# Kernel optimization log

Hardware: AMD Instinct MI355X
Metric: run time of the kernel (lower is better)

Reference implementation:

```python
import jax, jax.numpy as jnp
import numpy as np

OUT = 7        # out_size (H and W bins)
OUT_D = 4      # out_size_depth (D bins)
SCALE = 0.125  # spatial_scale (HW)
SCALE_D = 0.25 # spatial_scale_depth
SN = 2         # sample_num per bin per axis


def setup_inputs() -> dict:
    key = jax.random.key(0)
    k1, k2, k3, k4, k5 = jax.random.split(key, 5)
    N, C, D, H, W = 2, 128, 24, 128, 128
    features = jax.random.normal(k1, (N, C, D, H, W), dtype=jnp.float32)
    R = 256
    b = jax.random.randint(k2, (R,), 0, N).astype(jnp.float32)
    xx = jnp.sort(jax.random.uniform(k3, (R, 2), minval=0.0, maxval=1023.0), axis=1)
    yy = jnp.sort(jax.random.uniform(k4, (R, 2), minval=0.0, maxval=1023.0), axis=1)
    zz = jnp.sort(jax.random.uniform(k5, (R, 2), minval=0.0, maxval=95.0), axis=1)
    rois = jnp.stack([b, xx[:, 0], yy[:, 0], xx[:, 1], yy[:, 1], zz[:, 0], zz[:, 1]], axis=1)
    return {"features": features, "rois": rois}


def _axis(coord, dim):
    # mmcv-style clamping for (bi/tri)linear interpolation along one axis
    valid = (coord > -1.0) & (coord < dim)
    c = jnp.clip(coord, 0.0, dim - 1.0)
    low = jnp.minimum(jnp.floor(c).astype(jnp.int32), dim - 1)
    high = jnp.minimum(low + 1, dim - 1)
    frac = c - low.astype(coord.dtype)  # 0 when clamped at the top edge
    return low, high, frac, valid


def _roi_align_3d(features, rois):
    N, C, D, H, W = features.shape
    R = rois.shape[0]
    b = rois[:, 0].astype(jnp.int32)
    x1 = rois[:, 1] * SCALE
    y1 = rois[:, 2] * SCALE
    x2 = rois[:, 3] * SCALE
    y2 = rois[:, 4] * SCALE
    z1 = rois[:, 5] * SCALE_D
    z2 = rois[:, 6] * SCALE_D
    bw = jnp.maximum(x2 - x1, 1.0) / OUT
    bh = jnp.maximum(y2 - y1, 1.0) / OUT
    bd = jnp.maximum(z2 - z1, 1.0) / OUT_D

    off = (jnp.arange(SN, dtype=jnp.float32) + 0.5) / SN  # [SN]

    def coords(start, binsz, nbins):
        g = (jnp.arange(nbins, dtype=jnp.float32)[:, None] + off[None, :]).reshape(-1)  # [nbins*SN]
        return start[:, None] + g[None, :] * binsz[:, None]  # [R, nbins*SN]

    xs = coords(x1, bw, OUT)    # [R, Ws]
    ys = coords(y1, bh, OUT)    # [R, Hs]
    zs = coords(z1, bd, OUT_D)  # [R, Ds]

    zl, zh, fz, vz = _axis(zs, D)
    yl, yh, fy, vy = _axis(ys, H)
    xl, xh, fx, vx = _axis(xs, W)
    valid = (vz[:, :, None, None] & vy[:, None, :, None] & vx[:, None, None, :]).astype(features.dtype)

    Ds, Hs, Ws = OUT_D * SN, OUT * SN, OUT * SN
    acc = jnp.zeros((R, Ds, Hs, Ws, C), dtype=features.dtype)
    for zi, wz in ((zl, 1.0 - fz), (zh, fz)):
        for yi, wy in ((yl, 1.0 - fy), (yh, fy)):
            for xi, wx in ((xl, 1.0 - fx), (xh, fx)):
                w = wz[:, :, None, None] * wy[:, None, :, None] * wx[:, None, None, :] * valid
                # gather -> [R, Ds, Hs, Ws, C] (channel slice moves to the end)
                vals = features[b[:, None, None, None], :,
                                zi[:, :, None, None],
                                yi[:, None, :, None],
                                xi[:, None, None, :]]
                acc = acc + vals * w[..., None]

    # average the SN samples per bin along each axis
    out = acc.reshape(R, OUT_D, SN, OUT, SN, OUT, SN, C).mean(axis=(2, 4, 6))
    return jnp.transpose(out, (0, 4, 1, 2, 3))  # [R, C, OUT_D, OUT, OUT]


def reference(features, rois):
    return _roi_align_3d(features, rois)
```

## Files before the change

kernel.cpp:

```cpp
#include <hip/hip_runtime.h>


#define N_   2
#define C_   128
#define D_   24
#define H_   128
#define W_   128
#define OUTD 4
#define OUTHW 7

__device__ __forceinline__ void axis_sample(float coord, int dim,
                                            int& lo, int& hi,
                                            float& wlo, float& whi) {
    bool valid = (coord > -1.0f) && (coord < (float)dim);
    float c = fminf(fmaxf(coord, 0.0f), (float)(dim - 1));
    int l = (int)floorf(c);
    l = min(l, dim - 1);
    int h = min(l + 1, dim - 1);
    float f = c - (float)l;
    float v = valid ? 1.0f : 0.0f;
    lo = l; hi = h;
    wlo = (1.0f - f) * v;
    whi = f * v;
}

__global__ __launch_bounds__(256) void roialign3d_kernel(
    const float* __restrict__ feat,
    const float* __restrict__ rois,
    float* __restrict__ out,
    int total)
{
    unsigned idx = blockIdx.x * 256u + threadIdx.x;
    if ((int)idx >= total) return;

    unsigned t = idx;
    int pw = t % 7u;  t /= 7u;
    int ph = t % 7u;  t /= 7u;
    int pd = t % 4u;  t /= 4u;
    int c  = t % 128u;
    int r  = t / 128u;

    const float* roi = rois + r * 7;
    int   bi = (int)roi[0];
    float x1 = roi[1] * 0.125f;
    float y1 = roi[2] * 0.125f;
    float x2 = roi[3] * 0.125f;
    float y2 = roi[4] * 0.125f;
    float z1 = roi[5] * 0.25f;
    float z2 = roi[6] * 0.25f;
    float bw = fmaxf(x2 - x1, 1.0f) * (1.0f / 7.0f);
    float bh = fmaxf(y2 - y1, 1.0f) * (1.0f / 7.0f);
    float bd = fmaxf(z2 - z1, 1.0f) * (1.0f / 4.0f);

    int   zi_[4], yi_[4], xi_[4];
    float zw_[4], yw_[4], xw_[4];
#pragma unroll
    for (int s = 0; s < 2; ++s) {
        float off = (s == 0) ? 0.25f : 0.75f;
        int lo, hi; float wl, wh;

        axis_sample(z1 + ((float)pd + off) * bd, D_, lo, hi, wl, wh);
        zi_[2*s] = lo; zw_[2*s] = wl; zi_[2*s+1] = hi; zw_[2*s+1] = wh;

        axis_sample(y1 + ((float)ph + off) * bh, H_, lo, hi, wl, wh);
        yi_[2*s] = lo; yw_[2*s] = wl; yi_[2*s+1] = hi; yw_[2*s+1] = wh;

        axis_sample(x1 + ((float)pw + off) * bw, W_, lo, hi, wl, wh);
        xi_[2*s] = lo; xw_[2*s] = wl; xi_[2*s+1] = hi; xw_[2*s+1] = wh;
    }

    const float* fbase = feat + ((size_t)bi * C_ + c) * (size_t)(D_ * H_ * W_);

    float acc = 0.0f;
#pragma unroll
    for (int i = 0; i < 4; ++i) {
        float wz = zw_[i];
        if (wz != 0.0f) {
            int zo = zi_[i] * (H_ * W_);
#pragma unroll
            for (int j = 0; j < 4; ++j) {
                float wzy = wz * yw_[j];
                if (wzy != 0.0f) {
                    const float* row = fbase + zo + yi_[j] * W_;
                    float rs;
                    rs  = xw_[0] * row[xi_[0]];
                    rs += xw_[1] * row[xi_[1]];
                    rs += xw_[2] * row[xi_[2]];
                    rs += xw_[3] * row[xi_[3]];
                    acc += wzy * rs;
                }
            }
        }
    }

    out[idx] = acc * 0.125f;
}

extern "C" void kernel_launch(void* const* d_in, const int* in_sizes, int n_in,
                              void* d_out, int out_size, void* d_ws, size_t ws_size,
                              hipStream_t stream) {
    const float* feat = (const float*)d_in[0];
    const float* rois = (const float*)d_in[1];
    float* out = (float*)d_out;

    int total = out_size;
    int blocks = (total + 255) / 256;

    hipLaunchKernelGGL(roialign3d_kernel, dim3(blocks), dim3(256), 0, stream,
                       feat, rois, out, total);
}
```

Measured before the change: 783.5 us.

## Transpose features to channel-last fp16 then gather with vectorized channel loads

Adds a pre-pass that transposes the NCDHW fp32 features into a channels-last fp16 workspace. A new gather kernel then has each thread handle eight channels of one output cell, using 16-byte loads per trilinear corner. This replaces strided per-channel scalar gathers with contiguous loads. The cost is a full extra read and write of the feature tensor on every call, and fp16 storage reduces precision. It also drops the skipping of zero-weight corners, and falls back to the old direct kernel when the workspace is too small.

New measurement: 668.0 us. 1.17x faster.

```diff
diff --git a/kernel.cpp b/kernel.cpp
--- a/kernel.cpp
+++ b/kernel.cpp
@@ -1,4 +1,5 @@
 #include <hip/hip_runtime.h>
+#include <hip/hip_fp16.h>
 
 
 #define N_   2
@@ -6,8 +7,10 @@
 #define D_   24
 #define H_   128
 #define W_   128
-#define OUTD 4
-#define OUTHW 7
+#define HW_  (H_ * W_)
+#define DHW_ (D_ * H_ * W_)
+#define NVOX (N_ * D_ * H_ * W_)
+#define CELLS (256 * 4 * 7 * 7)
 
 __device__ __forceinline__ void axis_sample(float coord, int dim,
                                             int& lo, int& hi,
@@ -24,21 +27,59 @@
     whi = f * v;
 }
 
-__global__ __launch_bounds__(256) void roialign3d_kernel(
-    const float* __restrict__ feat,
-    const float* __restrict__ rois,
-    float* __restrict__ out,
-    int total)
+__global__ __launch_bounds__(256) void transpose_chlast_fp16(
+    const float* __restrict__ feat, unsigned short* __restrict__ ft)
 {
-    unsigned idx = blockIdx.x * 256u + threadIdx.x;
-    if ((int)idx >= total) return;
-
-    unsigned t = idx;
-    int pw = t % 7u;  t /= 7u;
-    int ph = t % 7u;  t /= 7u;
-    int pd = t % 4u;  t /= 4u;
-    int c  = t % 128u;
-    int r  = t / 128u;
+    __shared__ unsigned short lds[16][132];
+
+    int b  = blockIdx.x;
+    int xt = b & 7;
+    int y  = (b >> 3) & 127;
+    int zn = b >> 10;
+    int z  = zn % 24;
+    int n  = zn / 24;
+
+    int t  = threadIdx.x;
+    int x  = t & 15;
+    int c0 = t >> 4;
+
+    const float* src = feat + (size_t)(n * C_) * DHW_ + (size_t)z * HW_
+                            + y * W_ + xt * 16 + x;
+#pragma unroll
+    for (int p = 0; p < 8; ++p) {
+        int c = c0 + (p << 4);
+        float v = src[(size_t)c * DHW_];
+        lds[x][c] = __half_as_ushort(__float2half_rn(v));
+    }
+    __syncthreads();
+
+    int c2  = t & 63;
+    int xx0 = t >> 6;
+    size_t vox_base = (((size_t)(n * 24 + z) * 128 + y) * 128) + xt * 16;
+    ushort2* dst = (ushort2*)ft;
+#pragma unroll
+    for (int q = 0; q < 4; ++q) {
+        int xx = xx0 + (q << 2);
+        ushort2 val;
+        val.x = lds[xx][2 * c2];
+        val.y = lds[xx][2 * c2 + 1];
+        dst[(vox_base + xx) * 64 + c2] = val;
+    }
+}
+
+__global__ __launch_bounds__(256) void roialign_gather_fp16(
+    const unsigned short* __restrict__ ft, const float* __restrict__ rois,
+    float* __restrict__ out)
+{
+    int t = blockIdx.x * 256 + threadIdx.x;
+    int lane = t & 15;
+    int cell = t >> 4;
+    if (cell >= CELLS) return;
+
+    int pw = cell % 7;
+    int ph = (cell / 7) % 7;
+    int pd = (cell / 49) % 4;
+    int r  = cell / 196;
 
     const float* roi = rois + r * 7;
     int   bi = (int)roi[0];
@@ -69,14 +110,88 @@
         xi_[2*s] = lo; xw_[2*s] = wl; xi_[2*s+1] = hi; xw_[2*s+1] = wh;
     }
 
-    const float* fbase = feat + ((size_t)bi * C_ + c) * (size_t)(D_ * H_ * W_);
-
+    float acc[8] = {0.f, 0.f, 0.f, 0.f, 0.f, 0.f, 0.f, 0.f};
+    const unsigned short* basep = ft + (lane << 3);
+
+#pragma unroll
+    for (int i = 0; i < 4; ++i) {
+        int zrow = (bi * D_ + zi_[i]) * H_;
+        float wz = zw_[i];
+#pragma unroll
+        for (int j = 0; j < 4; ++j) {
+            float wzy = wz * yw_[j];
+            int yrow = (zrow + yi_[j]) * W_;
+#pragma unroll
+            for (int k = 0; k < 4; ++k) {
+                float w = wzy * xw_[k];
+                const unsigned short* p = basep + ((size_t)(yrow + xi_[k]) << 7);
+                uint4 u = *reinterpret_cast<const uint4*>(p);
+                float2 f0 = __half22float2(*reinterpret_cast<__half2*>(&u.x));
+                float2 f1 = __half22float2(*reinterpret_cast<__half2*>(&u.y));
+                float2 f2 = __half22float2(*reinterpret_cast<__half2*>(&u.z));
+                float2 f3 = __half22float2(*reinterpret_cast<__half2*>(&u.w));
+                acc[0] = fmaf(w, f0.x, acc[0]);
+                acc[1] = fmaf(w, f0.y, acc[1]);
+                acc[2] = fmaf(w, f1.x, acc[2]);
+                acc[3] = fmaf(w, f1.y, acc[3]);
+                acc[4] = fmaf(w, f2.x, acc[4]);
+                acc[5] = fmaf(w, f2.y, acc[5]);
+                acc[6] = fmaf(w, f3.x, acc[6]);
+                acc[7] = fmaf(w, f3.y, acc[7]);
+            }
+        }
+    }
+
+    int sp = (pd * 49 + ph * 7 + pw);
+    size_t ob = ((size_t)r * 128 + (lane << 3)) * 196 + sp;
+#pragma unroll
+    for (int j = 0; j < 8; ++j)
+        out[ob + (size_t)j * 196] = acc[j] * 0.125f;
+}
+
+__global__ __launch_bounds__(256) void roialign3d_direct(
+    const float* __restrict__ feat, const float* __restrict__ rois,
+    float* __restrict__ out, int total)
+{
+    unsigned idx = blockIdx.x * 256u + threadIdx.x;
+    if ((int)idx >= total) return;
+    unsigned t = idx;
+    int pw = t % 7u;  t /= 7u;
+    int ph = t % 7u;  t /= 7u;
+    int pd = t % 4u;  t /= 4u;
+    int c  = t % 128u;
+    int r  = t / 128u;
+
+    const float* roi = rois + r * 7;
+    int   bi = (int)roi[0];
+    float x1 = roi[1] * 0.125f, y1 = roi[2] * 0.125f;
+    float x2 = roi[3] * 0.125f, y2 = roi[4] * 0.125f;
+    float z1 = roi[5] * 0.25f,  z2 = roi[6] * 0.25f;
+    float bw = fmaxf(x2 - x1, 1.0f) * (1.0f / 7.0f);
+    float bh = fmaxf(y2 - y1, 1.0f) * (1.0f / 7.0f);
+    float bd = fmaxf(z2 - z1, 1.0f) * (1.0f / 4.0f);
+
+    int   zi_[4], yi_[4], xi_[4];
+    float zw_[4], yw_[4], xw_[4];
+#pragma unroll
+    for (int s = 0; s < 2; ++s) {
+        float off = (s == 0) ? 0.25f : 0.75f;
+        int lo, hi; float wl, wh;
+        axis_sample(z1 + ((float)pd + off) * bd, D_, lo, hi, wl, wh);
+        zi_[2*s] = lo; zw_[2*s] = wl; zi_[2*s+1] = hi; zw_[2*s+1] = wh;
+        axis_sample(y1 + ((float)ph + off) * bh, H_, lo, hi, wl, wh);
+        yi_[2*s] = lo; yw_[2*s] = wl; yi_[2*s+1] = hi; yw_[2*s+1] = wh;
+        axis_sample(x1 + ((float)pw + off) * bw, W_, lo, hi, wl, wh);
+        xi_[2*s] = lo; xw_[2*s] = wl; xi_[2*s+1] = hi; xw_[2*s+1] = wh;
+    }
+
+    const float* fbase = feat + ((size_t)bi * C_ + c) * (size_t)DHW_;
     float acc = 0.0f;
 #pragma unroll
     for (int i = 0; i < 4; ++i) {
         float wz = zw_[i];
         if (wz != 0.0f) {
-            int zo = zi_[i] * (H_ * W_);
+            int zo = zi_[i] * HW_;
 #pragma unroll
             for (int j = 0; j < 4; ++j) {
                 float wzy = wz * yw_[j];
@@ -92,7 +207,6 @@
             }
         }
     }
-
     out[idx] = acc * 0.125f;
 }
 
@@ -103,9 +217,18 @@
     const float* rois = (const float*)d_in[1];
     float* out = (float*)d_out;
 
-    int total = out_size;
-    int blocks = (total + 255) / 256;
-
-    hipLaunchKernelGGL(roialign3d_kernel, dim3(blocks), dim3(256), 0, stream,
-                       feat, rois, out, total);
-}
+    const size_t need = (size_t)NVOX * C_ * sizeof(unsigned short);
+
+    if (ws_size >= need) {
+        unsigned short* ft = (unsigned short*)d_ws;
+        hipLaunchKernelGGL(transpose_chlast_fp16, dim3(49152), dim3(256), 0, stream,
+                           feat, ft);
+        hipLaunchKernelGGL(roialign_gather_fp16, dim3(3136), dim3(256), 0, stream,
+                           ft, rois, out);
+    } else {
+        int total = out_size;
+        int blocks = (total + 255) / 256;
+        hipLaunchKernelGGL(roialign3d_direct, dim3(blocks), dim3(256), 0, stream,
+                           feat, rois, out, total);
+    }
+}
```
